# Optimization experiments

Measured on AMD Instinct MI355X. Metric: run time of the kernel, lower is better.

## Reference

```python
import jax, jax.numpy as jnp
import numpy as np

N_NODES = 100000
N_EDGES = 1600000
NUM_FEATURES = 128
HIDDEN = 128


def _linear_init(key, fan_in, fan_out):
    kw, kb = jax.random.split(key)
    bound = 1.0 / np.sqrt(fan_in)
    w = jax.random.uniform(kw, (fan_in, fan_out), jnp.float32, -bound, bound)
    b = jax.random.uniform(kb, (fan_out,), jnp.float32, -bound, bound)
    return w, b


def setup_inputs() -> dict:
    key = jax.random.key(0)
    ks = jax.random.split(key, 8)
    x = jax.random.normal(ks[0], (N_NODES, NUM_FEATURES), jnp.float32)
    edge_index = jax.random.randint(ks[1], (2, N_EDGES), 0, N_NODES, jnp.int64)
    w11, b11 = _linear_init(ks[2], NUM_FEATURES, HIDDEN)
    w12, b12 = _linear_init(ks[3], HIDDEN, HIDDEN)
    w21, b21 = _linear_init(ks[4], HIDDEN, HIDDEN)
    w22, b22 = _linear_init(ks[5], HIDDEN, HIDDEN)
    w31, b31 = _linear_init(ks[6], HIDDEN, HIDDEN)
    w32, b32 = _linear_init(ks[7], HIDDEN, 1)
    return {"x": x, "edge_index": edge_index,
            "w11": w11, "b11": b11, "w12": w12, "b12": b12,
            "w21": w21, "b21": b21, "w22": w22, "b22": b22,
            "w31": w31, "b31": b31, "w32": w32, "b32": b32}


def _gin_conv(x, src, dst, w1, b1, w2, b2):
    # GINConv (eps=0): h_i = MLP(x_i + sum_{j->i} x_j)
    agg = jax.ops.segment_sum(x[src], dst, num_segments=N_NODES)
    h = x + agg
    h = jax.nn.relu(h @ w1 + b1)
    return h @ w2 + b2


def reference(x, edge_index, w11, b11, w12, b12, w21, b21, w22, b22, w31, b31, w32, b32):
    src, dst = edge_index[0], edge_index[1]
    h = _gin_conv(x, src, dst, w11, b11, w12, b12)
    h = _gin_conv(h, src, dst, w21, b21, w22, b22)
    h = _gin_conv(h, src, dst, w31, b31, w32, b32)  # [N, 1]
    return h
```

## Files before the change

### kernel.cpp

```cpp
#include <hip/hip_runtime.h>

#define NN 100000
#define NE 1600000
#define F 128
#define NBUCK ((NN + 255) >> 8)
#define SCAT_BLOCKS 512
#define EPB (NE / SCAT_BLOCKS)
#define TROWS 128
#define NTILE ((NN + TROWS - 1) / TROWS)
#define IDX_CAP2 2816

typedef _Float16 f16x8 __attribute__((ext_vector_type(8)));
typedef float    f32x4 __attribute__((ext_vector_type(4)));
typedef unsigned short ushort8v __attribute__((ext_vector_type(8)));
typedef unsigned short ushort4v __attribute__((ext_vector_type(4)));

__device__ inline unsigned short f2h(float f) {
    _Float16 h = (_Float16)f;
    return __builtin_bit_cast(unsigned short, h);
}
__device__ inline float h2f(unsigned short u) {
    return (float)__builtin_bit_cast(_Float16, u);
}

__global__ __launch_bounds__(256) void k_bhist(const int* __restrict__ dst, int* __restrict__ bcnt) {
    __shared__ int sc[NBUCK];
    for (int i = threadIdx.x; i < NBUCK; i += 256) sc[i] = 0;
    __syncthreads();
    int stride = gridDim.x * 256;
    for (int e = blockIdx.x * 256 + threadIdx.x; e < NE; e += stride)
        atomicAdd(&sc[dst[e] >> 8], 1);
    __syncthreads();
    for (int i = threadIdx.x; i < NBUCK; i += 256) {
        int c = sc[i];
        if (c) atomicAdd(&bcnt[i], c);
    }
}

__global__ void k_bscan(const int* __restrict__ bcnt, int* __restrict__ bbase, int* __restrict__ bcur) {
    __shared__ int s[512];
    int t = threadIdx.x;
    int v = (t < NBUCK) ? bcnt[t] : 0;
    s[t] = v;
    __syncthreads();
    for (int off = 1; off < 512; off <<= 1) {
        int u = (t >= off) ? s[t - off] : 0;
        __syncthreads();
        s[t] += u;
        __syncthreads();
    }
    int excl = s[t] - v;
    if (t < NBUCK) { bbase[t] = excl; bcur[t] = excl; }
    if (t == 0) bbase[NBUCK] = NE;
}

__global__ __launch_bounds__(256) void k_scatterA(const int* __restrict__ src,
                                                  const int* __restrict__ dst,
                                                  int* __restrict__ bcur,
                                                  unsigned* __restrict__ scratch) {
    __shared__ uint2 sEdge[EPB];
    __shared__ int cnt[512];
    __shared__ int scn[512];
    __shared__ int cntB[512];
    __shared__ int gbase[512];
    __shared__ int ssum[256];

    const int tid = threadIdx.x;
    const int ebase = blockIdx.x * EPB;

#pragma unroll
    for (int i = tid; i < 512; i += 256) { cnt[i] = 0; cntB[i] = 0; }
    __syncthreads();

    for (int i = tid; i < EPB; i += 256) {
        int b = dst[ebase + i] >> 8;
        atomicAdd(&cnt[b], 1);
    }
    __syncthreads();

    int c0 = cnt[2 * tid], c1 = cnt[2 * tid + 1];
    ssum[tid] = c0 + c1;
    __syncthreads();
    for (int off = 1; off < 256; off <<= 1) {
        int v = (tid >= off) ? ssum[tid - off] : 0;
        __syncthreads();
        ssum[tid] += v;
        __syncthreads();
    }
    int texcl = (tid == 0) ? 0 : ssum[tid - 1];
    scn[2 * tid] = texcl;
    scn[2 * tid + 1] = texcl + c0;
#pragma unroll
    for (int i = tid; i < NBUCK; i += 256) {
        int c = cnt[i];
        gbase[i] = c ? atomicAdd(&bcur[i], c) : 0;
    }
    __syncthreads();

    for (int i = tid; i < EPB; i += 256) {
        int s = src[ebase + i], d = dst[ebase + i];
        int b = d >> 8;
        int rank = atomicAdd(&cntB[b], 1);
        sEdge[scn[b] + rank] = make_uint2((unsigned)s, (unsigned)d);
    }
    __syncthreads();

    for (int i = tid; i < EPB; i += 256) {
        uint2 ed = sEdge[i];
        int b = (int)(ed.y >> 8);
        unsigned w = ((ed.y & 255u) << 24) | ed.x;
        scratch[gbase[b] + (i - scn[b])] = w;
    }
}

__global__ __launch_bounds__(256) void k_fillB(const int* __restrict__ bbase,
                                               const unsigned* __restrict__ scratch,
                                               int* __restrict__ row_ptr,
                                               int* __restrict__ csr) {
    __shared__ int cnt[256];
    __shared__ int s[256];
    __shared__ int cur[256];
    int b = blockIdx.x;
    int base = bbase[b], end = bbase[b + 1];
    int t = threadIdx.x;
    cnt[t] = 0;
    __syncthreads();
    for (int i = base + t; i < end; i += 256)
        atomicAdd(&cnt[scratch[i] >> 24], 1);
    __syncthreads();
    int v = cnt[t];
    s[t] = v;
    __syncthreads();
    for (int off = 1; off < 256; off <<= 1) {
        int u = (t >= off) ? s[t - off] : 0;
        __syncthreads();
        s[t] += u;
        __syncthreads();
    }
    int excl = s[t] - v;
    int node = (b << 8) + t;
    if (node < NN) row_ptr[node] = base + excl;
    if (b == NBUCK - 1 && t == 0) row_ptr[NN] = NE;
    cur[t] = excl;
    __syncthreads();
    for (int i = base + t; i < end; i += 256) {
        unsigned w = scratch[i];
        int n = w >> 24;
        int p = atomicAdd(&cur[n], 1);
        csr[base + p] = (int)(w & 0xFFFFFFu);
    }
}

__global__ __launch_bounds__(256) void k_x2h(const float* __restrict__ x, unsigned short* __restrict__ xh) {
    int j = blockIdx.x * 256 + threadIdx.x;
    int c = blockIdx.y;
    if (j >= NN) return;
    const float4* px = (const float4*)&x[(size_t)j * F + c * 16];
    float4 v0 = px[0], v1 = px[1], v2 = px[2], v3 = px[3];
    ushort8v h0, h1;
    h0[0] = f2h(v0.x); h0[1] = f2h(v0.y); h0[2] = f2h(v0.z); h0[3] = f2h(v0.w);
    h0[4] = f2h(v1.x); h0[5] = f2h(v1.y); h0[6] = f2h(v1.z); h0[7] = f2h(v1.w);
    h1[0] = f2h(v2.x); h1[1] = f2h(v2.y); h1[2] = f2h(v2.z); h1[3] = f2h(v2.w);
    h1[4] = f2h(v3.x); h1[5] = f2h(v3.y); h1[6] = f2h(v3.z); h1[7] = f2h(v3.w);
    unsigned short* o = &xh[((size_t)c * NN + j) * 16];
    *(ushort8v*)o = h0;
    *(ushort8v*)(o + 8) = h1;
}

struct WPack {
    const float* w[5];
    unsigned short* t[5];
};

__global__ void k_w2h(WPack p) {
    int which = blockIdx.x >> 6;
    int idx = (blockIdx.x & 63) * 256 + threadIdx.x;
    int n = idx >> 7, k = idx & 127;
    p.t[which][idx] = f2h(p.w[which][k * 128 + n]);
}

template <bool LOC>
__device__ __forceinline__ void accum1(float a[8], int st, int e,
                                       const int* __restrict__ sIdx,
                                       const int* __restrict__ gIdx,
                                       const unsigned short* __restrict__ Gc,
                                       int lofs) {
    int p = st;
    for (; p + 4 <= e; p += 4) {
        int j0 = LOC ? sIdx[p]     : gIdx[p];
        int j1 = LOC ? sIdx[p + 1] : gIdx[p + 1];
        int j2 = LOC ? sIdx[p + 2] : gIdx[p + 2];
        int j3 = LOC ? sIdx[p + 3] : gIdx[p + 3];
        ushort8v v0 = *(const ushort8v*)&Gc[(size_t)j0 * 16 + lofs];
        ushort8v v1 = *(const ushort8v*)&Gc[(size_t)j1 * 16 + lofs];
        ushort8v v2 = *(const ushort8v*)&Gc[(size_t)j2 * 16 + lofs];
        ushort8v v3 = *(const ushort8v*)&Gc[(size_t)j3 * 16 + lofs];
#pragma unroll
        for (int k = 0; k < 8; ++k)
            a[k] += (h2f(v0[k]) + h2f(v1[k])) + (h2f(v2[k]) + h2f(v3[k]));
    }
    for (; p < e; ++p) {
        int j0 = LOC ? sIdx[p] : gIdx[p];
        ushort8v v0 = *(const ushort8v*)&Gc[(size_t)j0 * 16 + lofs];
#pragma unroll
        for (int k = 0; k < 8; ++k) a[k] += h2f(v0[k]);
    }
}

__global__ __launch_bounds__(256, 8) void k_agg(const unsigned short* __restrict__ G,
                                                const int* __restrict__ row_ptr,
                                                const int* __restrict__ csr,
                                                unsigned short* __restrict__ AGG) {
    __shared__ int sRP[TROWS + 1];
    __shared__ int sIdx[IDX_CAP2];

    const int tid  = threadIdx.x;
    const int tile = blockIdx.x >> 3;
    const int c    = blockIdx.x & 7;
    const int row0 = tile * TROWS;
    const unsigned short* Gc = G   + (size_t)c * NN * 16;
    unsigned short*       Ac = AGG + (size_t)c * NN * 16;

    if (tid < TROWS + 1) {
        int n = row0 + tid;
        if (n > NN) n = NN;
        sRP[tid] = row_ptr[n];
    }
    __syncthreads();
    const int ibase = sRP[0];
    const int icnt  = sRP[TROWS] - ibase;
    const int icap  = icnt < IDX_CAP2 ? icnt : IDX_CAP2;
    for (int i = tid; i < icap; i += 256) sIdx[i] = csr[ibase + i];
    __syncthreads();

    const int g    = tid >> 1;
    const int lofs = (tid & 1) * 8;
    const int node = row0 + g;
    if (node >= NN) return;

    float a[8];
    ushort8v sh = *(const ushort8v*)&Gc[(size_t)node * 16 + lofs];
#pragma unroll
    for (int k = 0; k < 8; ++k) a[k] = h2f(sh[k]);

    int st = sRP[g] - ibase, e = sRP[g + 1] - ibase;
    if (e <= icap)
        accum1<true>(a, st, e, sIdx, csr + ibase, Gc, lofs);
    else
        accum1<false>(a, st, e, sIdx, csr + ibase, Gc, lofs);

    ushort8v o;
#pragma unroll
    for (int k = 0; k < 8; ++k) o[k] = f2h(a[k]);
    *(ushort8v*)&Ac[(size_t)node * 16 + lofs] = o;
}

template <int L3>
__global__ __launch_bounds__(256, 6) void k_mlp(const unsigned short* __restrict__ AGG,
                                                const unsigned short* __restrict__ W1,
                                                const float* __restrict__ b1,
                                                const unsigned short* __restrict__ W2,
                                                const float* __restrict__ b2,
                                                const float* __restrict__ w32,
                                                const float* __restrict__ b32,
                                                unsigned short* __restrict__ H,
                                                float* __restrict__ out) {
    __shared__ __align__(16) unsigned short sA[64 * 128];

    const int tid = threadIdx.x;
    const int row0 = blockIdx.x * 64;
    const int cg   = tid >> 6;
    const int lane = tid & 63;
    const int m16  = lane & 15;
    const int quad = lane >> 4;

#pragma unroll
    for (int i = 0; i < 4; ++i) {
        int unit = i * 256 + tid;
        int c    = unit >> 7;
        int idx  = unit & 127;
        int node = idx >> 1;
        int h    = idx & 1;
        ushort8v v = {};
        if (row0 + node < NN)
            v = *(const ushort8v*)&AGG[((size_t)c * NN + row0 + node) * 16 + h * 8];
        int u = c * 2 + h;
        *(ushort8v*)&sA[node * 128 + ((u ^ (node & 15)) << 3)] = v;
    }
    __syncthreads();

    f32x4 acc[4][2] = {};
#pragma unroll
    for (int ks = 0; ks < 4; ++ks) {
        f16x8 a[4];
#pragma unroll
        for (int rt = 0; rt < 4; ++rt) {
            int rowL = rt * 16 + m16;
            int u = ks * 4 + quad;
            a[rt] = *(const f16x8*)&sA[rowL * 128 + ((u ^ (rowL & 15)) << 3)];
        }
#pragma unroll
        for (int ct = 0; ct < 2; ++ct) {
            int widx = (cg * 32 + ct * 16 + m16) * 128 + ks * 32 + quad * 8;
            f16x8 b = *(const f16x8*)&W1[widx];
#pragma unroll
            for (int rt = 0; rt < 4; ++rt)
                acc[rt][ct] = __builtin_amdgcn_mfma_f32_16x16x32_f16(a[rt], b, acc[rt][ct], 0, 0, 0);
        }
    }

    if (L3) {
        float* psf = (float*)sA;
        __syncthreads();
#pragma unroll
        for (int rt = 0; rt < 4; ++rt) {
            float s[4] = {0.f, 0.f, 0.f, 0.f};
#pragma unroll
            for (int ct = 0; ct < 2; ++ct) {
                int col = cg * 32 + ct * 16 + m16;
                float bv = b1[col];
                float wv = w32[col];
#pragma unroll
                for (int i = 0; i < 4; ++i) {
                    float v = fmaxf(acc[rt][ct][i] + bv, 0.f);
                    s[i] += v * wv;
                }
            }
#pragma unroll
            for (int i = 0; i < 4; ++i) {
#pragma unroll
                for (int mask = 1; mask < 16; mask <<= 1)
                    s[i] += __shfl_xor(s[i], mask, 64);
            }
            if (m16 == 0) {
#pragma unroll
                for (int i = 0; i < 4; ++i) {
                    int rowL = rt * 16 + quad * 4 + i;
                    psf[rowL * 4 + cg] = s[i];
                }
            }
        }
        __syncthreads();
        if (tid < 64) {
            int row = row0 + tid;
            if (row < NN)
                out[row] = (psf[tid * 4] + psf[tid * 4 + 1]) + (psf[tid * 4 + 2] + psf[tid * 4 + 3]) + b32[0];
        }
        return;
    }

    __syncthreads();
#pragma unroll
    for (int rt = 0; rt < 4; ++rt) {
#pragma unroll
        for (int ct = 0; ct < 2; ++ct) {
            int col = cg * 32 + ct * 16 + m16;
            float bv = b1[col];
#pragma unroll
            for (int i = 0; i < 4; ++i) {
                int rL = rt * 16 + quad * 4 + i;
                float v = fmaxf(acc[rt][ct][i] + bv, 0.f);
                sA[rL * 128 + (((col >> 3) ^ (rL & 15)) << 3) + (col & 7)] = f2h(v);
            }
        }
    }
    __syncthreads();

    f32x4 acc2[4][2] = {};
#pragma unroll
    for (int ks = 0; ks < 4; ++ks) {
        f16x8 a[4];
#pragma unroll
        for (int rt = 0; rt < 4; ++rt) {
            int rowL = rt * 16 + m16;
            int u = ks * 4 + quad;
            a[rt] = *(const f16x8*)&sA[rowL * 128 + ((u ^ (rowL & 15)) << 3)];
        }
#pragma unroll
        for (int ct = 0; ct < 2; ++ct) {
            int widx = (cg * 32 + ct * 16 + m16) * 128 + ks * 32 + quad * 8;
            f16x8 b = *(const f16x8*)&W2[widx];
#pragma unroll
            for (int rt = 0; rt < 4; ++rt)
                acc2[rt][ct] = __builtin_amdgcn_mfma_f32_16x16x32_f16(a[rt], b, acc2[rt][ct], 0, 0, 0);
        }
    }

    __syncthreads();
#pragma unroll
    for (int rt = 0; rt < 4; ++rt) {
#pragma unroll
        for (int ct = 0; ct < 2; ++ct) {
            int col = cg * 32 + ct * 16 + m16;
            float bv = b2[col];
#pragma unroll
            for (int i = 0; i < 4; ++i) {
                int rL = rt * 16 + quad * 4 + i;
                float v = acc2[rt][ct][i] + bv;
                sA[rL * 128 + (((col >> 3) ^ (rL & 15)) << 3) + (col & 7)] = f2h(v);
            }
        }
    }
    __syncthreads();
    {
#pragma unroll
        for (int i = 0; i < 4; ++i) {
            int unit = i * 256 + tid;
            int c    = unit >> 7;
            int idx  = unit & 127;
            int node = idx >> 1;
            int h    = idx & 1;
            int u    = c * 2 + h;
            if (row0 + node < NN)
                *(ushort8v*)&H[((size_t)c * NN + row0 + node) * 16 + h * 8] =
                    *(const ushort8v*)&sA[node * 128 + ((u ^ (node & 15)) << 3)];
        }
    }
}

static inline size_t align256(size_t x) { return (x + 255) & ~(size_t)255; }

extern "C" void kernel_launch(void* const* d_in, const int* in_sizes, int n_in,
                              void* d_out, int out_size, void* d_ws, size_t ws_size,
                              hipStream_t stream) {
    const float* x   = (const float*)d_in[0];
    const int*   ei  = (const int*)d_in[1];
    const float* w11 = (const float*)d_in[2];
    const float* b11 = (const float*)d_in[3];
    const float* w12 = (const float*)d_in[4];
    const float* b12 = (const float*)d_in[5];
    const float* w21 = (const float*)d_in[6];
    const float* b21 = (const float*)d_in[7];
    const float* w22 = (const float*)d_in[8];
    const float* b22 = (const float*)d_in[9];
    const float* w31 = (const float*)d_in[10];
    const float* b31 = (const float*)d_in[11];
    const float* w32 = (const float*)d_in[12];
    const float* b32 = (const float*)d_in[13];
    float* out = (float*)d_out;

    const int* src = ei;
    const int* dst = ei + NE;

    char* ws = (char*)d_ws;
    size_t off = 0;
    unsigned short* Abuf = (unsigned short*)(ws + off); off += align256((size_t)NN * F * 2);
    unsigned short* Bbuf = (unsigned short*)(ws + off); off += align256((size_t)NN * F * 2);
    unsigned short* AGG  = (unsigned short*)(ws + off); off += align256((size_t)NN * F * 2);
    int* bcnt    = (int*)(ws + off); off += align256((size_t)NBUCK * 4);
    int* bbase   = (int*)(ws + off); off += align256((size_t)(NBUCK + 1) * 4);
    int* bcur    = (int*)(ws + off); off += align256((size_t)NBUCK * 4);
    int* row_ptr = (int*)(ws + off); off += align256((size_t)(NN + 1) * 4);
    int* csr     = (int*)(ws + off); off += align256((size_t)NE * 4);
    unsigned* scratch = (unsigned*)(ws + off); off += align256((size_t)NE * 4);
    unsigned short* wt[5];
    for (int i = 0; i < 5; ++i) {
        wt[i] = (unsigned short*)(ws + off); off += align256((size_t)128 * 128 * 2);
    }
    (void)ws_size;

    WPack wp;
    wp.w[0] = w11; wp.w[1] = w12; wp.w[2] = w21; wp.w[3] = w22; wp.w[4] = w31;
    for (int i = 0; i < 5; ++i) wp.t[i] = wt[i];
    k_w2h<<<320, 256, 0, stream>>>(wp);
    {
        dim3 gx((NN + 255) / 256, 8);
        k_x2h<<<gx, 256, 0, stream>>>(x, Abuf);
    }

    (void)hipMemsetAsync(bcnt, 0, (size_t)NBUCK * 4, stream);
    k_bhist<<<256, 256, 0, stream>>>(dst, bcnt);
    k_bscan<<<1, 512, 0, stream>>>(bcnt, bbase, bcur);
    k_scatterA<<<SCAT_BLOCKS, 256, 0, stream>>>(src, dst, bcur, scratch);
    k_fillB<<<NBUCK, 256, 0, stream>>>(bbase, scratch, row_ptr, csr);

    const int mlpTiles = (NN + 63) / 64;
    const int aggBlocks = NTILE * 8;

    k_agg<<<aggBlocks, 256, 0, stream>>>(Abuf, row_ptr, csr, AGG);
    k_mlp<0><<<mlpTiles, 256, 0, stream>>>(AGG, wt[0], b11, wt[1], b12,
                                           nullptr, nullptr, Bbuf, nullptr);
    k_agg<<<aggBlocks, 256, 0, stream>>>(Bbuf, row_ptr, csr, AGG);
    k_mlp<0><<<mlpTiles, 256, 0, stream>>>(AGG, wt[2], b21, wt[3], b22,
                                           nullptr, nullptr, Abuf, nullptr);
    k_agg<<<aggBlocks, 256, 0, stream>>>(Abuf, row_ptr, csr, AGG);
    k_mlp<1><<<mlpTiles, 256, 0, stream>>>(AGG, wt[4], b31, nullptr, nullptr,
                                           w32, b32, nullptr, out);
}
```

Before: 473.1 us.

## Split aggregation by source-node half into partial sums with 32-wide feature chunks

Feature chunks widen from 16 to 32 halves (4 chunks instead of 8). Each aggregation block now handles one chunk and one half of the source-node range, skipping gathers from the other half, and writes a partial sum to a doubled PART buffer. The MLP adds the two partials while loading. The goal is to shrink each block's gather working set so it fits in cache better. The cost is twice the partial-sum write and read traffic, predicated loads that still walk every edge index, and an extra fp16 rounding when the partials are combined.

```diff
diff --git a/kernel.cpp b/kernel.cpp
--- a/kernel.cpp
+++ b/kernel.cpp
@@ -3,12 +3,13 @@
 #define NN 100000
 #define NE 1600000
 #define F 128
+#define HALFN 50000
 #define NBUCK ((NN + 255) >> 8)
 #define SCAT_BLOCKS 512
 #define EPB (NE / SCAT_BLOCKS)
-#define TROWS 128
+#define TROWS 64
 #define NTILE ((NN + TROWS - 1) / TROWS)
-#define IDX_CAP2 2816
+#define IDX_CAP 1536
 
 typedef _Float16 f16x8 __attribute__((ext_vector_type(8)));
 typedef float    f32x4 __attribute__((ext_vector_type(4)));
@@ -155,16 +156,16 @@
     int j = blockIdx.x * 256 + threadIdx.x;
     int c = blockIdx.y;
     if (j >= NN) return;
-    const float4* px = (const float4*)&x[(size_t)j * F + c * 16];
-    float4 v0 = px[0], v1 = px[1], v2 = px[2], v3 = px[3];
-    ushort8v h0, h1;
-    h0[0] = f2h(v0.x); h0[1] = f2h(v0.y); h0[2] = f2h(v0.z); h0[3] = f2h(v0.w);
-    h0[4] = f2h(v1.x); h0[5] = f2h(v1.y); h0[6] = f2h(v1.z); h0[7] = f2h(v1.w);
-    h1[0] = f2h(v2.x); h1[1] = f2h(v2.y); h1[2] = f2h(v2.z); h1[3] = f2h(v2.w);
-    h1[4] = f2h(v3.x); h1[5] = f2h(v3.y); h1[6] = f2h(v3.z); h1[7] = f2h(v3.w);
-    unsigned short* o = &xh[((size_t)c * NN + j) * 16];
-    *(ushort8v*)o = h0;
-    *(ushort8v*)(o + 8) = h1;
+    const float4* px = (const float4*)&x[(size_t)j * F + c * 32];
+    unsigned short* o = &xh[((size_t)c * NN + j) * 32];
+#pragma unroll
+    for (int half = 0; half < 4; ++half) {
+        float4 v0 = px[half * 2], v1 = px[half * 2 + 1];
+        ushort8v h;
+        h[0] = f2h(v0.x); h[1] = f2h(v0.y); h[2] = f2h(v0.z); h[3] = f2h(v0.w);
+        h[4] = f2h(v1.x); h[5] = f2h(v1.y); h[6] = f2h(v1.z); h[7] = f2h(v1.w);
+        *(ushort8v*)(o + half * 8) = h;
+    }
 }
 
 struct WPack {
@@ -180,46 +181,50 @@
 }
 
 template <bool LOC>
-__device__ __forceinline__ void accum1(float a[8], int st, int e,
-                                       const int* __restrict__ sIdx,
-                                       const int* __restrict__ gIdx,
-                                       const unsigned short* __restrict__ Gc,
-                                       int lofs) {
+__device__ __forceinline__ void accum_half(float a[8], int st, int e,
+                                           const int* __restrict__ sIdx,
+                                           const int* __restrict__ gIdx,
+                                           const unsigned short* __restrict__ Gc,
+                                           int lofs, bool hb) {
     int p = st;
     for (; p + 4 <= e; p += 4) {
         int j0 = LOC ? sIdx[p]     : gIdx[p];
         int j1 = LOC ? sIdx[p + 1] : gIdx[p + 1];
         int j2 = LOC ? sIdx[p + 2] : gIdx[p + 2];
         int j3 = LOC ? sIdx[p + 3] : gIdx[p + 3];
-        ushort8v v0 = *(const ushort8v*)&Gc[(size_t)j0 * 16 + lofs];
-        ushort8v v1 = *(const ushort8v*)&Gc[(size_t)j1 * 16 + lofs];
-        ushort8v v2 = *(const ushort8v*)&Gc[(size_t)j2 * 16 + lofs];
-        ushort8v v3 = *(const ushort8v*)&Gc[(size_t)j3 * 16 + lofs];
+        ushort8v v0 = {}, v1 = {}, v2 = {}, v3 = {};
+        if ((j0 >= HALFN) == hb) v0 = *(const ushort8v*)&Gc[(size_t)j0 * 32 + lofs];
+        if ((j1 >= HALFN) == hb) v1 = *(const ushort8v*)&Gc[(size_t)j1 * 32 + lofs];
+        if ((j2 >= HALFN) == hb) v2 = *(const ushort8v*)&Gc[(size_t)j2 * 32 + lofs];
+        if ((j3 >= HALFN) == hb) v3 = *(const ushort8v*)&Gc[(size_t)j3 * 32 + lofs];
 #pragma unroll
         for (int k = 0; k < 8; ++k)
             a[k] += (h2f(v0[k]) + h2f(v1[k])) + (h2f(v2[k]) + h2f(v3[k]));
     }
     for (; p < e; ++p) {
         int j0 = LOC ? sIdx[p] : gIdx[p];
-        ushort8v v0 = *(const ushort8v*)&Gc[(size_t)j0 * 16 + lofs];
-#pragma unroll
-        for (int k = 0; k < 8; ++k) a[k] += h2f(v0[k]);
+        if ((j0 >= HALFN) == hb) {
+            ushort8v v0 = *(const ushort8v*)&Gc[(size_t)j0 * 32 + lofs];
+#pragma unroll
+            for (int k = 0; k < 8; ++k) a[k] += h2f(v0[k]);
+        }
     }
 }
 
 __global__ __launch_bounds__(256, 8) void k_agg(const unsigned short* __restrict__ G,
                                                 const int* __restrict__ row_ptr,
                                                 const int* __restrict__ csr,
-                                                unsigned short* __restrict__ AGG) {
+                                                unsigned short* __restrict__ PART) {
     __shared__ int sRP[TROWS + 1];
-    __shared__ int sIdx[IDX_CAP2];
+    __shared__ int sIdx[IDX_CAP];
 
     const int tid  = threadIdx.x;
     const int tile = blockIdx.x >> 3;
-    const int c    = blockIdx.x & 7;
+    const int cc   = blockIdx.x & 7;
+    const int c    = cc & 3;
+    const bool hb  = (cc >> 2) != 0;
     const int row0 = tile * TROWS;
-    const unsigned short* Gc = G   + (size_t)c * NN * 16;
-    unsigned short*       Ac = AGG + (size_t)c * NN * 16;
+    const unsigned short* Gc = G + (size_t)c * NN * 32;
 
     if (tid < TROWS + 1) {
         int n = row0 + tid;
@@ -229,34 +234,36 @@
     __syncthreads();
     const int ibase = sRP[0];
     const int icnt  = sRP[TROWS] - ibase;
-    const int icap  = icnt < IDX_CAP2 ? icnt : IDX_CAP2;
+    const int icap  = icnt < IDX_CAP ? icnt : IDX_CAP;
     for (int i = tid; i < icap; i += 256) sIdx[i] = csr[ibase + i];
     __syncthreads();
 
-    const int g    = tid >> 1;
-    const int lofs = (tid & 1) * 8;
+    const int g    = tid >> 2;
+    const int lofs = (tid & 3) * 8;
     const int node = row0 + g;
     if (node >= NN) return;
 
-    float a[8];
-    ushort8v sh = *(const ushort8v*)&Gc[(size_t)node * 16 + lofs];
-#pragma unroll
-    for (int k = 0; k < 8; ++k) a[k] = h2f(sh[k]);
+    float a[8] = {};
+    if ((node >= HALFN) == hb) {
+        ushort8v sh = *(const ushort8v*)&Gc[(size_t)node * 32 + lofs];
+#pragma unroll
+        for (int k = 0; k < 8; ++k) a[k] = h2f(sh[k]);
+    }
 
     int st = sRP[g] - ibase, e = sRP[g + 1] - ibase;
     if (e <= icap)
-        accum1<true>(a, st, e, sIdx, csr + ibase, Gc, lofs);
+        accum_half<true>(a, st, e, sIdx, csr + ibase, Gc, lofs, hb);
     else
-        accum1<false>(a, st, e, sIdx, csr + ibase, Gc, lofs);
+        accum_half<false>(a, st, e, sIdx, csr + ibase, Gc, lofs, hb);
 
     ushort8v o;
 #pragma unroll
     for (int k = 0; k < 8; ++k) o[k] = f2h(a[k]);
-    *(ushort8v*)&Ac[(size_t)node * 16 + lofs] = o;
+    *(ushort8v*)&PART[((size_t)cc * NN + node) * 32 + lofs] = o;
 }
 
 template <int L3>
-__global__ __launch_bounds__(256, 6) void k_mlp(const unsigned short* __restrict__ AGG,
+__global__ __launch_bounds__(256, 6) void k_mlp(const unsigned short* __restrict__ PART,
                                                 const unsigned short* __restrict__ W1,
                                                 const float* __restrict__ b1,
                                                 const unsigned short* __restrict__ W2,
@@ -273,19 +280,25 @@
     const int lane = tid & 63;
     const int m16  = lane & 15;
     const int quad = lane >> 4;
+    const size_t H1OFF = (size_t)4 * NN * 32;
 
 #pragma unroll
     for (int i = 0; i < 4; ++i) {
         int unit = i * 256 + tid;
-        int c    = unit >> 7;
-        int idx  = unit & 127;
-        int node = idx >> 1;
-        int h    = idx & 1;
-        ushort8v v = {};
-        if (row0 + node < NN)
-            v = *(const ushort8v*)&AGG[((size_t)c * NN + row0 + node) * 16 + h * 8];
-        int u = c * 2 + h;
-        *(ushort8v*)&sA[node * 128 + ((u ^ (node & 15)) << 3)] = v;
+        int c    = unit >> 8;
+        int idx  = unit & 255;
+        int node = idx >> 2;
+        int q    = idx & 3;
+        ushort8v o = {};
+        if (row0 + node < NN) {
+            size_t base = ((size_t)c * NN + row0 + node) * 32 + q * 8;
+            ushort8v v0 = *(const ushort8v*)&PART[base];
+            ushort8v v1 = *(const ushort8v*)&PART[H1OFF + base];
+#pragma unroll
+            for (int k = 0; k < 8; ++k) o[k] = f2h(h2f(v0[k]) + h2f(v1[k]));
+        }
+        int u = c * 4 + q;
+        *(ushort8v*)&sA[node * 128 + ((u ^ (node & 15)) << 3)] = o;
     }
     __syncthreads();
 
@@ -406,13 +419,13 @@
 #pragma unroll
         for (int i = 0; i < 4; ++i) {
             int unit = i * 256 + tid;
-            int c    = unit >> 7;
-            int idx  = unit & 127;
-            int node = idx >> 1;
-            int h    = idx & 1;
-            int u    = c * 2 + h;
+            int c    = unit >> 8;
+            int idx  = unit & 255;
+            int node = idx >> 2;
+            int q    = idx & 3;
+            int u    = c * 4 + q;
             if (row0 + node < NN)
-                *(ushort8v*)&H[((size_t)c * NN + row0 + node) * 16 + h * 8] =
+                *(ushort8v*)&H[((size_t)c * NN + row0 + node) * 32 + q * 8] =
                     *(const ushort8v*)&sA[node * 128 + ((u ^ (node & 15)) << 3)];
         }
     }
@@ -446,7 +459,7 @@
     size_t off = 0;
     unsigned short* Abuf = (unsigned short*)(ws + off); off += align256((size_t)NN * F * 2);
     unsigned short* Bbuf = (unsigned short*)(ws + off); off += align256((size_t)NN * F * 2);
-    unsigned short* AGG  = (unsigned short*)(ws + off); off += align256((size_t)NN * F * 2);
+    unsigned short* PART = (unsigned short*)(ws + off); off += align256((size_t)NN * F * 2 * 2);
     int* bcnt    = (int*)(ws + off); off += align256((size_t)NBUCK * 4);
     int* bbase   = (int*)(ws + off); off += align256((size_t)(NBUCK + 1) * 4);
     int* bcur    = (int*)(ws + off); off += align256((size_t)NBUCK * 4);
@@ -464,12 +477,12 @@
     for (int i = 0; i < 5; ++i) wp.t[i] = wt[i];
     k_w2h<<<320, 256, 0, stream>>>(wp);
     {
-        dim3 gx((NN + 255) / 256, 8);
+        dim3 gx((NN + 255) / 256, 4);
         k_x2h<<<gx, 256, 0, stream>>>(x, Abuf);
     }
 
     (void)hipMemsetAsync(bcnt, 0, (size_t)NBUCK * 4, stream);
-    k_bhist<<<256, 256, 0, stream>>>(dst, bcnt);
+    k_bhist<<<512, 256, 0, stream>>>(dst, bcnt);
     k_bscan<<<1, 512, 0, stream>>>(bcnt, bbase, bcur);
     k_scatterA<<<SCAT_BLOCKS, 256, 0, stream>>>(src, dst, bcur, scratch);
     k_fillB<<<NBUCK, 256, 0, stream>>>(bbase, scratch, row_ptr, csr);
@@ -477,13 +490,13 @@
     const int mlpTiles = (NN + 63) / 64;
     const int aggBlocks = NTILE * 8;
 
-    k_agg<<<aggBlocks, 256, 0, stream>>>(Abuf, row_ptr, csr, AGG);
-    k_mlp<0><<<mlpTiles, 256, 0, stream>>>(AGG, wt[0], b11, wt[1], b12,
+    k_agg<<<aggBlocks, 256, 0, stream>>>(Abuf, row_ptr, csr, PART);
+    k_mlp<0><<<mlpTiles, 256, 0, stream>>>(PART, wt[0], b11, wt[1], b12,
                                            nullptr, nullptr, Bbuf, nullptr);
-    k_agg<<<aggBlocks, 256, 0, stream>>>(Bbuf, row_ptr, csr, AGG);
-    k_mlp<0><<<mlpTiles, 256, 0, stream>>>(AGG, wt[2], b21, wt[3], b22,
+    k_agg<<<aggBlocks, 256, 0, stream>>>(Bbuf, row_ptr, csr, PART);
+    k_mlp<0><<<mlpTiles, 256, 0, stream>>>(PART, wt[2], b21, wt[3], b22,
                                            nullptr, nullptr, Abuf, nullptr);
-    k_agg<<<aggBlocks, 256, 0, stream>>>(Abuf, row_ptr, csr, AGG);
-    k_mlp<1><<<mlpTiles, 256, 0, stream>>>(AGG, wt[4], b31, nullptr, nullptr,
+    k_agg<<<aggBlocks, 256, 0, stream>>>(Abuf, row_ptr, csr, PART);
+    k_mlp<1><<<mlpTiles, 256, 0, stream>>>(PART, wt[4], b31, nullptr, nullptr,
                                            w32, b32, nullptr, out);
 }
```

Result: no change. 464.3 us (-1.9%).
